# Performance work log

Measured on AMD Instinct MI355X. Metric: run time of the kernel, lower is better.

Reference implementation:

```python
import jax, jax.numpy as jnp
import numpy as np

B, S, D = 8, 4096, 1280   # batch, tokens, model width (== down_dim == out_dim)
R = 64                    # lora rank (mid_dim)
EMBED_W = D + R * R + D   # [down | mid | up] slices of the per-sample embed


def setup_inputs() -> dict:
    key = jax.random.key(0)
    ks = jax.random.split(key, 6)
    x = jax.random.normal(ks[0], (B, S, D), dtype=jnp.float32)
    embed = jax.random.normal(ks[1], (B, EMBED_W), dtype=jnp.float32) * 0.05
    w_down = jax.random.normal(ks[2], (R, D), dtype=jnp.float32) * 0.02
    b_down = jnp.zeros((R,), dtype=jnp.float32)
    w_up = jax.random.normal(ks[3], (D, R), dtype=jnp.float32) * 0.02
    b_up = jnp.zeros((D,), dtype=jnp.float32)
    return {"x": x, "embed": embed, "w_down": w_down, "b_down": b_down,
            "w_up": w_up, "b_up": b_up}


def reference(x, embed, w_down, b_down, w_up, b_up):
    # down_forward: modulate input channels by per-sample down weight, then lora_down
    down_w = embed[:, :D]                          # [B, D]
    h = x * down_w[:, None, :]                     # [B, S, D]
    h = jnp.einsum('bsd,rd->bsr', h, w_down) + b_down   # lora_down Linear(D->R)
    # mid_forward: per-sample [R,R] weight, x_chunk @ W.T  (batched, no python loop)
    mid_w = embed[:, D:D + R * R].reshape(B, R, R)       # [B, R, R]
    h = jnp.einsum('bsr,bqr->bsq', h, mid_w)             # [B, S, R]
    # up_forward: lora_up then modulate output channels by per-sample up weight
    out = jnp.einsum('bsr,dr->bsd', h, w_up) + b_up      # lora_up Linear(R->D)
    up_w = embed[:, -D:]                                 # [B, D]
    out = out * up_w[:, None, :]
    return out
```

## Files before the change

kernel.cpp:

```cpp
#include <hip/hip_runtime.h>

#define NB 8
#define NS 4096
#define ND 1280
#define NR 64
#define EW 6656

typedef __attribute__((ext_vector_type(4))) float f4;
typedef __attribute__((ext_vector_type(8))) short bf8;

__device__ __forceinline__ unsigned short f2bf(float f) {
  union { float f; unsigned u; } v; v.f = f;
  unsigned u = v.u + 0x7FFFu + ((v.u >> 16) & 1u);
  return (unsigned short)(u >> 16);
}

__global__ __launch_bounds__(256) void prep_all(const float* __restrict__ embed,
                                                const float* __restrict__ w_down,
                                                const float* __restrict__ w_up,
                                                const float* __restrict__ b_down,
                                                unsigned short* __restrict__ W2F,
                                                unsigned short* __restrict__ W3F,
                                                float* __restrict__ h2bias) {
  const int blk = blockIdx.x;
  const int t   = threadIdx.x;
  if (blk < 160) {
    const int b  = blk / 20;
    const int qg = (blk % 20) / 5;
    const int dg = blk % 5;
    __shared__ float mids[16][64];
    #pragma unroll
    for (int i = 0; i < 4; ++i) {
      int idx = t + i * 256;
      mids[idx >> 6][idx & 63] = embed[b * EW + ND + qg * 1024 + idx];
    }
    __syncthreads();
    const int d = dg * 256 + t;
    float acc[16];
    #pragma unroll
    for (int q = 0; q < 16; ++q) acc[q] = 0.f;
    for (int r = 0; r < 64; r += 8) {
      float wd[8];
      #pragma unroll
      for (int u = 0; u < 8; ++u) wd[u] = w_down[(r + u) * ND + d];
      #pragma unroll
      for (int u = 0; u < 8; ++u)
        #pragma unroll
        for (int q = 0; q < 16; ++q) acc[q] += mids[q][r + u] * wd[u];
    }
    const float dwn = embed[b * EW + d];
    const int kt = d >> 5, lanehi = (d & 31) >> 3, jj = d & 7;
    #pragma unroll
    for (int q = 0; q < 16; ++q)
      W2F[(((b * 40 + kt) * 4 + qg) << 9) + (lanehi * 16 + q) * 8 + jj] = f2bf(acc[q] * dwn);
  } else if (blk < 480) {
    int g = (blk - 160) * 256 + t;
    int d = g >> 6, q = g & 63;
    int kt = q >> 5, nt = d >> 4, lanei = ((q & 31) >> 3) * 16 + (d & 15), jj = q & 7;
    W3F[((kt * 80 + nt) * 64 + lanei) * 8 + jj] = f2bf(w_up[g]);
  } else {
    #pragma unroll
    for (int ii = 0; ii < 2; ++ii) {
      int id = ii * 256 + t;
      int bb = id >> 6, q = id & 63;
      float s = 0.f;
      for (int r = 0; r < 64; ++r) s += b_down[r] * embed[bb * EW + ND + q * 64 + r];
      h2bias[id] = s;
    }
  }
}

__global__ __launch_bounds__(256, 4) void fused_main(const float* __restrict__ x,
                                                     const float* __restrict__ embed,
                                                     const float* __restrict__ b_up,
                                                     const unsigned short* __restrict__ W2F,
                                                     const unsigned short* __restrict__ W3F,
                                                     const float* __restrict__ h2bias,
                                                     float* __restrict__ out) {
  const int tid  = threadIdx.x;
  const int lane = tid & 63;
  const int w    = tid >> 6;
  const int kh   = w >> 1;
  const int rt   = w & 1;
  const int b    = blockIdx.x & 7;
  const int tile = blockIdx.x >> 3;
  const int lo16 = lane & 15;
  const int hi4  = lane >> 4;
  const int wrow = tile * 32 + rt * 16;

  __shared__ __align__(16) char smem[32768 + 256];
  float (*xs)[2][1024]    = (float (*)[2][1024])smem;
  float (*h2p)[2][16][68] = (float (*)[2][16][68])smem;
  float* bias_s           = (float*)(smem + 32768);

  if (tid < 64) bias_s[tid] = h2bias[b * 64 + tid];

  const float* xbase = x + ((size_t)b * NS + wrow) * ND + kh * 640;
  const unsigned short* w2b = W2F + (size_t)b * 81920;

  #define ISSUE_DMA(ck, buf)                                                         \
    _Pragma("unroll")                                                                \
    for (int it = 0; it < 4; ++it) {                                                 \
      const int rloc = it * 4 + hi4;                                                 \
      const int cf   = lo16 ^ rloc;                                                  \
      const float* src = xbase + (size_t)rloc * ND + (ck) * 64 + cf * 4;             \
      __builtin_amdgcn_global_load_lds((__attribute__((address_space(1))) void*)src, \
          (__attribute__((address_space(3))) void*)&xs[w][buf][it * 256], 16, 0, 0); \
    }

  f4 acc[4] = {};
  bf8 bw[8];

  ISSUE_DMA(0, 0)
  {
    const unsigned short* wp = w2b + (((kh * 10) * 8) << 9) + lane * 8;
    #pragma unroll
    for (int i = 0; i < 8; ++i) bw[i] = *(const bf8*)(wp + (i << 9));
  }

  for (int ck = 0; ck < 10; ++ck) {
    const int buf = ck & 1;
    asm volatile("s_waitcnt vmcnt(0)" ::: "memory");
    const f4* xp = (const f4*)&xs[w][buf][0];
    f4 a0 = xp[lo16 * 16 + ((hi4 * 2)     ^ lo16)];
    f4 a1 = xp[lo16 * 16 + ((hi4 * 2 + 1) ^ lo16)];
    f4 a2 = xp[lo16 * 16 + ((hi4 * 2 + 8) ^ lo16)];
    f4 a3 = xp[lo16 * 16 + ((hi4 * 2 + 9) ^ lo16)];
    bf8 bn[8];
    const bool more = (ck < 9);
    if (more) {
      ISSUE_DMA(ck + 1, buf ^ 1)
      const unsigned short* wp = w2b + (size_t)(((kh * 10 + ck + 1) * 8) << 9) + lane * 8;
      #pragma unroll
      for (int i = 0; i < 8; ++i) bn[i] = *(const bf8*)(wp + (i << 9));
    }
    bf8 af0, af1;
    #pragma unroll
    for (int j = 0; j < 4; ++j) {
      af0[j]     = (short)f2bf(a0[j]);
      af0[4 + j] = (short)f2bf(a1[j]);
      af1[j]     = (short)f2bf(a2[j]);
      af1[4 + j] = (short)f2bf(a3[j]);
    }
    #pragma unroll
    for (int nt = 0; nt < 4; ++nt)
      acc[nt] = __builtin_amdgcn_mfma_f32_16x16x32_bf16(af0, bw[nt], acc[nt], 0, 0, 0);
    #pragma unroll
    for (int nt = 0; nt < 4; ++nt)
      acc[nt] = __builtin_amdgcn_mfma_f32_16x16x32_bf16(af1, bw[4 + nt], acc[nt], 0, 0, 0);
    if (more) {
      #pragma unroll
      for (int i = 0; i < 8; ++i) bw[i] = bn[i];
    }
  }

  __syncthreads();

  #pragma unroll
  for (int nt = 0; nt < 4; ++nt)
    #pragma unroll
    for (int j = 0; j < 4; ++j)
      h2p[kh][rt][hi4 * 4 + j][nt * 16 + lo16] = acc[nt][j];
  __syncthreads();

  const int row = lo16;
  f4 u0 = *(const f4*)&h2p[0][rt][row][hi4 * 8];
  f4 u1 = *(const f4*)&h2p[0][rt][row][hi4 * 8 + 4];
  f4 v0 = *(const f4*)&h2p[1][rt][row][hi4 * 8];
  f4 v1 = *(const f4*)&h2p[1][rt][row][hi4 * 8 + 4];
  f4 u2 = *(const f4*)&h2p[0][rt][row][32 + hi4 * 8];
  f4 u3 = *(const f4*)&h2p[0][rt][row][32 + hi4 * 8 + 4];
  f4 v2 = *(const f4*)&h2p[1][rt][row][32 + hi4 * 8];
  f4 v3 = *(const f4*)&h2p[1][rt][row][32 + hi4 * 8 + 4];
  bf8 ha0, ha1;
  #pragma unroll
  for (int j = 0; j < 4; ++j) {
    ha0[j]     = (short)f2bf(u0[j] + v0[j] + bias_s[hi4 * 8 + j]);
    ha0[4 + j] = (short)f2bf(u1[j] + v1[j] + bias_s[hi4 * 8 + 4 + j]);
    ha1[j]     = (short)f2bf(u2[j] + v2[j] + bias_s[32 + hi4 * 8 + j]);
    ha1[4 + j] = (short)f2bf(u3[j] + v3[j] + bias_s[32 + hi4 * 8 + 4 + j]);
  }

  const float* upw = embed + b * EW + (EW - ND);
  float* outp = out + ((size_t)b * NS + wrow + hi4 * 4) * ND;
  const int dt0 = kh * 40;
  bf8 b0 = *(const bf8*)(W3F + (size_t)(dt0 * 64 + lane) * 8);
  bf8 b1 = *(const bf8*)(W3F + (size_t)((80 + dt0) * 64 + lane) * 8);

  for (int i = 0; i < 40; ++i) {
    const int dt  = dt0 + i;
    const int pdt = (i < 39) ? dt + 1 : dt;
    bf8 nb0 = *(const bf8*)(W3F + (size_t)(pdt * 64 + lane) * 8);
    bf8 nb1 = *(const bf8*)(W3F + (size_t)((80 + pdt) * 64 + lane) * 8);
    f4 o = {};
    o = __builtin_amdgcn_mfma_f32_16x16x32_bf16(ha0, b0, o, 0, 0, 0);
    o = __builtin_amdgcn_mfma_f32_16x16x32_bf16(ha1, b1, o, 0, 0, 0);
    const int d = dt * 16 + lo16;
    const float scale = upw[d];
    const float bu = b_up[d];
    #pragma unroll
    for (int j = 0; j < 4; ++j)
      outp[(size_t)j * ND + d] = (o[j] + bu) * scale;
    b0 = nb0; b1 = nb1;
  }
}

extern "C" void kernel_launch(void* const* d_in, const int* in_sizes, int n_in,
                              void* d_out, int out_size, void* d_ws, size_t ws_size,
                              hipStream_t stream) {
  const float* x      = (const float*)d_in[0];
  const float* embed  = (const float*)d_in[1];
  const float* w_down = (const float*)d_in[2];
  const float* b_down = (const float*)d_in[3];
  const float* w_up   = (const float*)d_in[4];
  const float* b_up   = (const float*)d_in[5];
  float* out = (float*)d_out;

  unsigned short* W2F = (unsigned short*)d_ws;
  unsigned short* W3F = W2F + 8 * 40 * 4 * 512;
  float* h2bias = (float*)(W3F + 2 * 80 * 64 * 8);

  prep_all<<<481, 256, 0, stream>>>(embed, w_down, w_up, b_down, W2F, W3F, h2bias);
  fused_main<<<1024, 256, 0, stream>>>(x, embed, b_up, W2F, W3F, h2bias, out);
}
```

Before: 124.0 us.

## Split fused kernel into h2 projection and output kernels with coalesced stores

Splits the single fused kernel into two launches when workspace allows. The first computes the bf16 rank-64 intermediate and writes it to workspace. The second reloads it and runs the up-projection with transposed MFMA operands, staging results through LDS so each output row is written as coalesced 16-byte stores. It also swaps the hand-written bf16 rounding for packed float2-to-bf16 conversions. The aim is better store efficiency and occupancy for the write-heavy output phase, paid for with an extra launch and a workspace round trip for the intermediate.

```diff
diff --git a/kernel.cpp b/kernel.cpp
--- a/kernel.cpp
+++ b/kernel.cpp
@@ -1,4 +1,5 @@
 #include <hip/hip_runtime.h>
+#include <hip/hip_bf16.h>
 
 #define NB 8
 #define NS 4096
@@ -9,10 +10,17 @@
 typedef __attribute__((ext_vector_type(4))) float f4;
 typedef __attribute__((ext_vector_type(8))) short bf8;
 
+union BF8U { bf8 v; unsigned u[4]; };
+
 __device__ __forceinline__ unsigned short f2bf(float f) {
   union { float f; unsigned u; } v; v.f = f;
   unsigned u = v.u + 0x7FFFu + ((v.u >> 16) & 1u);
   return (unsigned short)(u >> 16);
+}
+
+__device__ __forceinline__ unsigned pk2(float a, float b) {
+  __hip_bfloat162 t = __float22bfloat162_rn(float2{a, b});
+  return *reinterpret_cast<unsigned*>(&t);
 }
 
 __global__ __launch_bounds__(256) void prep_all(const float* __restrict__ embed,
@@ -67,6 +75,185 @@
       for (int r = 0; r < 64; ++r) s += b_down[r] * embed[bb * EW + ND + q * 64 + r];
       h2bias[id] = s;
     }
+  }
+}
+
+__global__ __launch_bounds__(256) void k1_h2(const float* __restrict__ x,
+                                             const unsigned short* __restrict__ W2F,
+                                             const float* __restrict__ h2bias,
+                                             uint4* __restrict__ h2F) {
+  const int tid  = threadIdx.x;
+  const int lane = tid & 63;
+  const int w    = tid >> 6;
+  const int kh   = w >> 1;
+  const int rt   = w & 1;
+  const int b    = blockIdx.x & 7;
+  const int tile = blockIdx.x >> 3;
+  const int lo16 = lane & 15;
+  const int hi4  = lane >> 4;
+  const int wrow = tile * 32 + rt * 16;
+
+  __shared__ __align__(16) char smem[32768];
+  float (*xs)[2][1024]    = (float (*)[2][1024])smem;
+  float (*h2p)[2][16][68] = (float (*)[2][16][68])smem;
+
+  const float* xbase = x + ((size_t)b * NS + wrow) * ND + kh * 640;
+  const unsigned short* w2b = W2F + (size_t)b * 81920;
+
+  #define ISSUE_DMA(ck, buf)                                                         \
+    _Pragma("unroll")                                                                \
+    for (int it = 0; it < 4; ++it) {                                                 \
+      const int rloc = it * 4 + hi4;                                                 \
+      const int cf   = lo16 ^ rloc;                                                  \
+      const float* src = xbase + (size_t)rloc * ND + (ck) * 64 + cf * 4;             \
+      __builtin_amdgcn_global_load_lds((__attribute__((address_space(1))) void*)src, \
+          (__attribute__((address_space(3))) void*)&xs[w][buf][it * 256], 16, 0, 0); \
+    }
+
+  f4 acc[4] = {};
+  bf8 bw[8];
+
+  ISSUE_DMA(0, 0)
+  {
+    const unsigned short* wp = w2b + (((kh * 10) * 8) << 9) + lane * 8;
+    #pragma unroll
+    for (int i = 0; i < 8; ++i) bw[i] = *(const bf8*)(wp + (i << 9));
+  }
+
+  for (int ck = 0; ck < 10; ++ck) {
+    const int buf = ck & 1;
+    asm volatile("s_waitcnt vmcnt(0)" ::: "memory");
+    const f4* xp = (const f4*)&xs[w][buf][0];
+    f4 a0 = xp[lo16 * 16 + ((hi4 * 2)     ^ lo16)];
+    f4 a1 = xp[lo16 * 16 + ((hi4 * 2 + 1) ^ lo16)];
+    f4 a2 = xp[lo16 * 16 + ((hi4 * 2 + 8) ^ lo16)];
+    f4 a3 = xp[lo16 * 16 + ((hi4 * 2 + 9) ^ lo16)];
+    bf8 bn[8];
+    const bool more = (ck < 9);
+    if (more) {
+      ISSUE_DMA(ck + 1, buf ^ 1)
+      const unsigned short* wp = w2b + (size_t)(((kh * 10 + ck + 1) * 8) << 9) + lane * 8;
+      #pragma unroll
+      for (int i = 0; i < 8; ++i) bn[i] = *(const bf8*)(wp + (i << 9));
+    }
+    BF8U af0, af1;
+    af0.u[0] = pk2(a0[0], a0[1]); af0.u[1] = pk2(a0[2], a0[3]);
+    af0.u[2] = pk2(a1[0], a1[1]); af0.u[3] = pk2(a1[2], a1[3]);
+    af1.u[0] = pk2(a2[0], a2[1]); af1.u[1] = pk2(a2[2], a2[3]);
+    af1.u[2] = pk2(a3[0], a3[1]); af1.u[3] = pk2(a3[2], a3[3]);
+    #pragma unroll
+    for (int nt = 0; nt < 4; ++nt)
+      acc[nt] = __builtin_amdgcn_mfma_f32_16x16x32_bf16(af0.v, bw[nt], acc[nt], 0, 0, 0);
+    #pragma unroll
+    for (int nt = 0; nt < 4; ++nt)
+      acc[nt] = __builtin_amdgcn_mfma_f32_16x16x32_bf16(af1.v, bw[4 + nt], acc[nt], 0, 0, 0);
+    if (more) {
+      #pragma unroll
+      for (int i = 0; i < 8; ++i) bw[i] = bn[i];
+    }
+  }
+
+  __syncthreads();
+
+  #pragma unroll
+  for (int nt = 0; nt < 4; ++nt)
+    #pragma unroll
+    for (int j = 0; j < 4; ++j)
+      h2p[kh][rt][hi4 * 4 + j][nt * 16 + lo16] = acc[nt][j];
+  __syncthreads();
+
+  const int q0 = kh * 32 + hi4 * 8;
+  f4 u0 = *(const f4*)&h2p[0][rt][lo16][q0];
+  f4 u1 = *(const f4*)&h2p[0][rt][lo16][q0 + 4];
+  f4 v0 = *(const f4*)&h2p[1][rt][lo16][q0];
+  f4 v1 = *(const f4*)&h2p[1][rt][lo16][q0 + 4];
+  f4 c0 = *(const f4*)(h2bias + b * 64 + q0);
+  f4 c1 = *(const f4*)(h2bias + b * 64 + q0 + 4);
+  float s[8];
+  #pragma unroll
+  for (int j = 0; j < 4; ++j) {
+    s[j]     = u0[j] + v0[j] + c0[j];
+    s[4 + j] = u1[j] + v1[j] + c1[j];
+  }
+  uint4 pk;
+  pk.x = pk2(s[0], s[1]); pk.y = pk2(s[2], s[3]);
+  pk.z = pk2(s[4], s[5]); pk.w = pk2(s[6], s[7]);
+  h2F[(size_t)(((b * 256 + tile * 2 + rt) * 2 + kh) * 64 + lane)] = pk;
+}
+
+__global__ __launch_bounds__(256) void k2_out(const uint4* __restrict__ h2F,
+                                              const float* __restrict__ embed,
+                                              const float* __restrict__ b_up,
+                                              const unsigned short* __restrict__ W3F,
+                                              float* __restrict__ out) {
+  const int tid  = threadIdx.x;
+  const int lane = tid & 63;
+  const int w    = tid >> 6;
+  const int kh   = w >> 1;
+  const int rt   = w & 1;
+  const int b    = blockIdx.x & 7;
+  const int t2   = blockIdx.x >> 3;
+  const int lo16 = lane & 15;
+  const int hi4  = lane >> 4;
+
+  __shared__ __align__(16) float lds[4][16][68];
+
+  const int tile16 = t2 * 2 + rt;
+  uint4 hv0 = h2F[(size_t)(((b * 256 + tile16) * 2 + 0) * 64 + lane)];
+  uint4 hv1 = h2F[(size_t)(((b * 256 + tile16) * 2 + 1) * 64 + lane)];
+  BF8U ha0, ha1;
+  ha0.u[0] = hv0.x; ha0.u[1] = hv0.y; ha0.u[2] = hv0.z; ha0.u[3] = hv0.w;
+  ha1.u[0] = hv1.x; ha1.u[1] = hv1.y; ha1.u[2] = hv1.z; ha1.u[3] = hv1.w;
+
+  const int d0 = kh * 640;
+  const float* upw = embed + b * EW + (EW - ND) + d0;
+  const float* bup = b_up + d0;
+  float* outp = out + ((size_t)b * NS + t2 * 32 + rt * 16) * ND + d0;
+  const int dtbase = kh * 40;
+
+  bf8 wb[4][2];
+  #pragma unroll
+  for (int i = 0; i < 4; ++i) {
+    const int dt = dtbase + i;
+    wb[i][0] = *(const bf8*)(W3F + (size_t)(dt * 64 + lane) * 8);
+    wb[i][1] = *(const bf8*)(W3F + (size_t)((80 + dt) * 64 + lane) * 8);
+  }
+
+  for (int c = 0; c < 10; ++c) {
+    f4 o[4];
+    #pragma unroll
+    for (int i = 0; i < 4; ++i) {
+      f4 t = {};
+      t = __builtin_amdgcn_mfma_f32_16x16x32_bf16(wb[i][0], ha0.v, t, 0, 0, 0);
+      t = __builtin_amdgcn_mfma_f32_16x16x32_bf16(wb[i][1], ha1.v, t, 0, 0, 0);
+      o[i] = t;
+    }
+    bf8 wn[4][2];
+    if (c < 9) {
+      #pragma unroll
+      for (int i = 0; i < 4; ++i) {
+        const int dt = dtbase + (c + 1) * 4 + i;
+        wn[i][0] = *(const bf8*)(W3F + (size_t)(dt * 64 + lane) * 8);
+        wn[i][1] = *(const bf8*)(W3F + (size_t)((80 + dt) * 64 + lane) * 8);
+      }
+    }
+    #pragma unroll
+    for (int i = 0; i < 4; ++i) {
+      const int dl = c * 64 + i * 16 + hi4 * 4;
+      f4 sc = *(const f4*)(upw + dl);
+      f4 bu = *(const f4*)(bup + dl);
+      f4 r;
+      #pragma unroll
+      for (int j = 0; j < 4; ++j) r[j] = (o[i][j] + bu[j]) * sc[j];
+      *(f4*)&lds[w][lo16][i * 16 + hi4 * 4] = r;
+    }
+    #pragma unroll
+    for (int k = 0; k < 4; ++k) {
+      f4 v = *(const f4*)&lds[w][4 * k + hi4][lo16 * 4];
+      *(f4*)(outp + (size_t)(4 * k + hi4) * ND + c * 64 + lo16 * 4) = v;
+    }
+    #pragma unroll
+    for (int i = 0; i < 4; ++i) { wb[i][0] = wn[i][0]; wb[i][1] = wn[i][1]; }
   }
 }
 
@@ -98,26 +285,14 @@
   const float* xbase = x + ((size_t)b * NS + wrow) * ND + kh * 640;
   const unsigned short* w2b = W2F + (size_t)b * 81920;
 
-  #define ISSUE_DMA(ck, buf)                                                         \
-    _Pragma("unroll")                                                                \
-    for (int it = 0; it < 4; ++it) {                                                 \
-      const int rloc = it * 4 + hi4;                                                 \
-      const int cf   = lo16 ^ rloc;                                                  \
-      const float* src = xbase + (size_t)rloc * ND + (ck) * 64 + cf * 4;             \
-      __builtin_amdgcn_global_load_lds((__attribute__((address_space(1))) void*)src, \
-          (__attribute__((address_space(3))) void*)&xs[w][buf][it * 256], 16, 0, 0); \
-    }
-
   f4 acc[4] = {};
   bf8 bw[8];
-
   ISSUE_DMA(0, 0)
   {
     const unsigned short* wp = w2b + (((kh * 10) * 8) << 9) + lane * 8;
     #pragma unroll
     for (int i = 0; i < 8; ++i) bw[i] = *(const bf8*)(wp + (i << 9));
   }
-
   for (int ck = 0; ck < 10; ++ck) {
     const int buf = ck & 1;
     asm volatile("s_waitcnt vmcnt(0)" ::: "memory");
@@ -134,35 +309,29 @@
       #pragma unroll
       for (int i = 0; i < 8; ++i) bn[i] = *(const bf8*)(wp + (i << 9));
     }
-    bf8 af0, af1;
-    #pragma unroll
-    for (int j = 0; j < 4; ++j) {
-      af0[j]     = (short)f2bf(a0[j]);
-      af0[4 + j] = (short)f2bf(a1[j]);
-      af1[j]     = (short)f2bf(a2[j]);
-      af1[4 + j] = (short)f2bf(a3[j]);
-    }
+    BF8U af0, af1;
+    af0.u[0] = pk2(a0[0], a0[1]); af0.u[1] = pk2(a0[2], a0[3]);
+    af0.u[2] = pk2(a1[0], a1[1]); af0.u[3] = pk2(a1[2], a1[3]);
+    af1.u[0] = pk2(a2[0], a2[1]); af1.u[1] = pk2(a2[2], a2[3]);
+    af1.u[2] = pk2(a3[0], a3[1]); af1.u[3] = pk2(a3[2], a3[3]);
     #pragma unroll
     for (int nt = 0; nt < 4; ++nt)
-      acc[nt] = __builtin_amdgcn_mfma_f32_16x16x32_bf16(af0, bw[nt], acc[nt], 0, 0, 0);
+      acc[nt] = __builtin_amdgcn_mfma_f32_16x16x32_bf16(af0.v, bw[nt], acc[nt], 0, 0, 0);
     #pragma unroll
     for (int nt = 0; nt < 4; ++nt)
-      acc[nt] = __builtin_amdgcn_mfma_f32_16x16x32_bf16(af1, bw[4 + nt], acc[nt], 0, 0, 0);
+      acc[nt] = __builtin_amdgcn_mfma_f32_16x16x32_bf16(af1.v, bw[4 + nt], acc[nt], 0, 0, 0);
     if (more) {
       #pragma unroll
       for (int i = 0; i < 8; ++i) bw[i] = bn[i];
     }
   }
-
   __syncthreads();
-
   #pragma unroll
   for (int nt = 0; nt < 4; ++nt)
     #pragma unroll
     for (int j = 0; j < 4; ++j)
       h2p[kh][rt][hi4 * 4 + j][nt * 16 + lo16] = acc[nt][j];
   __syncthreads();
-
   const int row = lo16;
   f4 u0 = *(const f4*)&h2p[0][rt][row][hi4 * 8];
   f4 u1 = *(const f4*)&h2p[0][rt][row][hi4 * 8 + 4];
@@ -180,13 +349,11 @@
     ha1[j]     = (short)f2bf(u2[j] + v2[j] + bias_s[32 + hi4 * 8 + j]);
     ha1[4 + j] = (short)f2bf(u3[j] + v3[j] + bias_s[32 + hi4 * 8 + 4 + j]);
   }
-
   const float* upw = embed + b * EW + (EW - ND);
   float* outp = out + ((size_t)b * NS + wrow + hi4 * 4) * ND;
   const int dt0 = kh * 40;
   bf8 b0 = *(const bf8*)(W3F + (size_t)(dt0 * 64 + lane) * 8);
   bf8 b1 = *(const bf8*)(W3F + (size_t)((80 + dt0) * 64 + lane) * 8);
-
   for (int i = 0; i < 40; ++i) {
     const int dt  = dt0 + i;
     const int pdt = (i < 39) ? dt + 1 : dt;
@@ -216,10 +383,18 @@
   const float* b_up   = (const float*)d_in[5];
   float* out = (float*)d_out;
 
-  unsigned short* W2F = (unsigned short*)d_ws;
-  unsigned short* W3F = W2F + 8 * 40 * 4 * 512;
-  float* h2bias = (float*)(W3F + 2 * 80 * 64 * 8);
+  char* ws = (char*)d_ws;
+  unsigned short* W2F = (unsigned short*)ws;
+  unsigned short* W3F = (unsigned short*)(ws + 1310720);
+  float* h2bias       = (float*)(ws + 1474560);
+  uint4* h2F          = (uint4*)(ws + 1476608);
+  const size_t need   = 1476608 + 4194304;
 
   prep_all<<<481, 256, 0, stream>>>(embed, w_down, w_up, b_down, W2F, W3F, h2bias);
-  fused_main<<<1024, 256, 0, stream>>>(x, embed, b_up, W2F, W3F, h2bias, out);
-}
+  if (ws_size >= need) {
+    k1_h2 <<<1024, 256, 0, stream>>>(x, W2F, h2bias, h2F);
+    k2_out<<<1024, 256, 0, stream>>>(h2F, embed, b_up, W3F, out);
+  } else {
+    fused_main<<<1024, 256, 0, stream>>>(x, embed, b_up, W2F, W3F, h2bias, out);
+  }
+}
```

Result: faster. 104.9 us (-15.4%).

## Split fused kernel into h2 and output kernels with pre-scaled up weights

Applied to the files above, without the earlier changes.

Splits the single fused kernel into two: one computes the bf16 rank-64 intermediate and writes it to workspace, and one runs the up-projection. The per-sample up scale is folded into a per-batch bf16 copy of w_up during prep, and the up bias times scale is staged in LDS. Output tiles are transposed through LDS so each row is written as contiguous 128-byte segments, in place of scattered scalar stores. It also relaxes the DMA wait to vmcnt(12) for overlap and uses packed bf16 conversion. The cost is an extra launch, an intermediate round trip through global memory, and a larger prep kernel.

```diff
diff --git a/kernel.cpp b/kernel.cpp
--- a/kernel.cpp
+++ b/kernel.cpp
@@ -1,4 +1,5 @@
 #include <hip/hip_runtime.h>
+#include <hip/hip_bf16.h>
 
 #define NB 8
 #define NS 4096
@@ -9,10 +10,17 @@
 typedef __attribute__((ext_vector_type(4))) float f4;
 typedef __attribute__((ext_vector_type(8))) short bf8;
 
+union BF8U { bf8 v; unsigned u[4]; };
+
 __device__ __forceinline__ unsigned short f2bf(float f) {
   union { float f; unsigned u; } v; v.f = f;
   unsigned u = v.u + 0x7FFFu + ((v.u >> 16) & 1u);
   return (unsigned short)(u >> 16);
+}
+
+__device__ __forceinline__ unsigned pk2(float a, float b) {
+  __hip_bfloat162 t = __float22bfloat162_rn(float2{a, b});
+  return *reinterpret_cast<unsigned*>(&t);
 }
 
 __global__ __launch_bounds__(256) void prep_all(const float* __restrict__ embed,
@@ -20,7 +28,7 @@
                                                 const float* __restrict__ w_up,
                                                 const float* __restrict__ b_down,
                                                 unsigned short* __restrict__ W2F,
-                                                unsigned short* __restrict__ W3F,
+                                                unsigned short* __restrict__ W3FB,
                                                 float* __restrict__ h2bias) {
   const int blk = blockIdx.x;
   const int t   = threadIdx.x;
@@ -53,11 +61,15 @@
     #pragma unroll
     for (int q = 0; q < 16; ++q)
       W2F[(((b * 40 + kt) * 4 + qg) << 9) + (lanehi * 16 + q) * 8 + jj] = f2bf(acc[q] * dwn);
-  } else if (blk < 480) {
-    int g = (blk - 160) * 256 + t;
-    int d = g >> 6, q = g & 63;
-    int kt = q >> 5, nt = d >> 4, lanei = ((q & 31) >> 3) * 16 + (d & 15), jj = q & 7;
-    W3F[((kt * 80 + nt) * 64 + lanei) * 8 + jj] = f2bf(w_up[g]);
+  } else if (blk < 2720) {
+    const int local = blk - 160;
+    const int b  = local / 320;
+    const int g  = (local % 320) * 256 + t;
+    const int d  = g >> 6, q = g & 63;
+    const int kt = q >> 5, nt = d >> 4;
+    const int lanei = ((q & 31) >> 3) * 16 + (d & 15), jj = q & 7;
+    const float upw = embed[b * EW + 5376 + d];
+    W3FB[(size_t)b * 81920 + ((kt * 80 + nt) * 64 + lanei) * 8 + jj] = f2bf(w_up[g] * upw);
   } else {
     #pragma unroll
     for (int ii = 0; ii < 2; ++ii) {
@@ -70,13 +82,10 @@
   }
 }
 
-__global__ __launch_bounds__(256, 4) void fused_main(const float* __restrict__ x,
-                                                     const float* __restrict__ embed,
-                                                     const float* __restrict__ b_up,
-                                                     const unsigned short* __restrict__ W2F,
-                                                     const unsigned short* __restrict__ W3F,
-                                                     const float* __restrict__ h2bias,
-                                                     float* __restrict__ out) {
+__global__ __launch_bounds__(256, 4) void k1_h2(const float* __restrict__ x,
+                                                const unsigned short* __restrict__ W2F,
+                                                const float* __restrict__ h2bias,
+                                                uint4* __restrict__ h2F) {
   const int tid  = threadIdx.x;
   const int lane = tid & 63;
   const int w    = tid >> 6;
@@ -88,12 +97,9 @@
   const int hi4  = lane >> 4;
   const int wrow = tile * 32 + rt * 16;
 
-  __shared__ __align__(16) char smem[32768 + 256];
+  __shared__ __align__(16) char smem[32768];
   float (*xs)[2][1024]    = (float (*)[2][1024])smem;
   float (*h2p)[2][16][68] = (float (*)[2][16][68])smem;
-  float* bias_s           = (float*)(smem + 32768);
-
-  if (tid < 64) bias_s[tid] = h2bias[b * 64 + tid];
 
   const float* xbase = x + ((size_t)b * NS + wrow) * ND + kh * 640;
   const unsigned short* w2b = W2F + (size_t)b * 81920;
@@ -120,35 +126,33 @@
 
   for (int ck = 0; ck < 10; ++ck) {
     const int buf = ck & 1;
-    asm volatile("s_waitcnt vmcnt(0)" ::: "memory");
+    bf8 bn[8];
+    if (ck < 9) {
+      ISSUE_DMA(ck + 1, buf ^ 1)
+      const unsigned short* wp = w2b + (size_t)(((kh * 10 + ck + 1) * 8) << 9) + lane * 8;
+      #pragma unroll
+      for (int i = 0; i < 8; ++i) bn[i] = *(const bf8*)(wp + (i << 9));
+      asm volatile("s_waitcnt vmcnt(12)" ::: "memory");
+    } else {
+      asm volatile("s_waitcnt vmcnt(0)" ::: "memory");
+    }
     const f4* xp = (const f4*)&xs[w][buf][0];
     f4 a0 = xp[lo16 * 16 + ((hi4 * 2)     ^ lo16)];
     f4 a1 = xp[lo16 * 16 + ((hi4 * 2 + 1) ^ lo16)];
     f4 a2 = xp[lo16 * 16 + ((hi4 * 2 + 8) ^ lo16)];
     f4 a3 = xp[lo16 * 16 + ((hi4 * 2 + 9) ^ lo16)];
-    bf8 bn[8];
-    const bool more = (ck < 9);
-    if (more) {
-      ISSUE_DMA(ck + 1, buf ^ 1)
-      const unsigned short* wp = w2b + (size_t)(((kh * 10 + ck + 1) * 8) << 9) + lane * 8;
-      #pragma unroll
-      for (int i = 0; i < 8; ++i) bn[i] = *(const bf8*)(wp + (i << 9));
-    }
-    bf8 af0, af1;
-    #pragma unroll
-    for (int j = 0; j < 4; ++j) {
-      af0[j]     = (short)f2bf(a0[j]);
-      af0[4 + j] = (short)f2bf(a1[j]);
-      af1[j]     = (short)f2bf(a2[j]);
-      af1[4 + j] = (short)f2bf(a3[j]);
-    }
+    BF8U af0, af1;
+    af0.u[0] = pk2(a0[0], a0[1]); af0.u[1] = pk2(a0[2], a0[3]);
+    af0.u[2] = pk2(a1[0], a1[1]); af0.u[3] = pk2(a1[2], a1[3]);
+    af1.u[0] = pk2(a2[0], a2[1]); af1.u[1] = pk2(a2[2], a2[3]);
+    af1.u[2] = pk2(a3[0], a3[1]); af1.u[3] = pk2(a3[2], a3[3]);
     #pragma unroll
     for (int nt = 0; nt < 4; ++nt)
-      acc[nt] = __builtin_amdgcn_mfma_f32_16x16x32_bf16(af0, bw[nt], acc[nt], 0, 0, 0);
+      acc[nt] = __builtin_amdgcn_mfma_f32_16x16x32_bf16(af0.v, bw[nt], acc[nt], 0, 0, 0);
     #pragma unroll
     for (int nt = 0; nt < 4; ++nt)
-      acc[nt] = __builtin_amdgcn_mfma_f32_16x16x32_bf16(af1, bw[4 + nt], acc[nt], 0, 0, 0);
-    if (more) {
+      acc[nt] = __builtin_amdgcn_mfma_f32_16x16x32_bf16(af1.v, bw[4 + nt], acc[nt], 0, 0, 0);
+    if (ck < 9) {
       #pragma unroll
       for (int i = 0; i < 8; ++i) bw[i] = bn[i];
     }
@@ -163,45 +167,97 @@
       h2p[kh][rt][hi4 * 4 + j][nt * 16 + lo16] = acc[nt][j];
   __syncthreads();
 
-  const int row = lo16;
-  f4 u0 = *(const f4*)&h2p[0][rt][row][hi4 * 8];
-  f4 u1 = *(const f4*)&h2p[0][rt][row][hi4 * 8 + 4];
-  f4 v0 = *(const f4*)&h2p[1][rt][row][hi4 * 8];
-  f4 v1 = *(const f4*)&h2p[1][rt][row][hi4 * 8 + 4];
-  f4 u2 = *(const f4*)&h2p[0][rt][row][32 + hi4 * 8];
-  f4 u3 = *(const f4*)&h2p[0][rt][row][32 + hi4 * 8 + 4];
-  f4 v2 = *(const f4*)&h2p[1][rt][row][32 + hi4 * 8];
-  f4 v3 = *(const f4*)&h2p[1][rt][row][32 + hi4 * 8 + 4];
-  bf8 ha0, ha1;
+  const int q0 = kh * 32 + hi4 * 8;
+  f4 u0 = *(const f4*)&h2p[0][rt][lo16][q0];
+  f4 u1 = *(const f4*)&h2p[0][rt][lo16][q0 + 4];
+  f4 v0 = *(const f4*)&h2p[1][rt][lo16][q0];
+  f4 v1 = *(const f4*)&h2p[1][rt][lo16][q0 + 4];
+  f4 c0 = *(const f4*)(h2bias + b * 64 + q0);
+  f4 c1 = *(const f4*)(h2bias + b * 64 + q0 + 4);
+  float s[8];
   #pragma unroll
   for (int j = 0; j < 4; ++j) {
-    ha0[j]     = (short)f2bf(u0[j] + v0[j] + bias_s[hi4 * 8 + j]);
-    ha0[4 + j] = (short)f2bf(u1[j] + v1[j] + bias_s[hi4 * 8 + 4 + j]);
-    ha1[j]     = (short)f2bf(u2[j] + v2[j] + bias_s[32 + hi4 * 8 + j]);
-    ha1[4 + j] = (short)f2bf(u3[j] + v3[j] + bias_s[32 + hi4 * 8 + 4 + j]);
-  }
-
-  const float* upw = embed + b * EW + (EW - ND);
-  float* outp = out + ((size_t)b * NS + wrow + hi4 * 4) * ND;
-  const int dt0 = kh * 40;
-  bf8 b0 = *(const bf8*)(W3F + (size_t)(dt0 * 64 + lane) * 8);
-  bf8 b1 = *(const bf8*)(W3F + (size_t)((80 + dt0) * 64 + lane) * 8);
-
-  for (int i = 0; i < 40; ++i) {
-    const int dt  = dt0 + i;
-    const int pdt = (i < 39) ? dt + 1 : dt;
-    bf8 nb0 = *(const bf8*)(W3F + (size_t)(pdt * 64 + lane) * 8);
-    bf8 nb1 = *(const bf8*)(W3F + (size_t)((80 + pdt) * 64 + lane) * 8);
-    f4 o = {};
-    o = __builtin_amdgcn_mfma_f32_16x16x32_bf16(ha0, b0, o, 0, 0, 0);
-    o = __builtin_amdgcn_mfma_f32_16x16x32_bf16(ha1, b1, o, 0, 0, 0);
-    const int d = dt * 16 + lo16;
-    const float scale = upw[d];
-    const float bu = b_up[d];
-    #pragma unroll
-    for (int j = 0; j < 4; ++j)
-      outp[(size_t)j * ND + d] = (o[j] + bu) * scale;
-    b0 = nb0; b1 = nb1;
+    s[j]     = u0[j] + v0[j] + c0[j];
+    s[4 + j] = u1[j] + v1[j] + c1[j];
+  }
+  uint4 pk;
+  pk.x = pk2(s[0], s[1]); pk.y = pk2(s[2], s[3]);
+  pk.z = pk2(s[4], s[5]); pk.w = pk2(s[6], s[7]);
+  h2F[(size_t)(((b * 256 + tile * 2 + rt) * 2 + kh) * 64 + lane)] = pk;
+}
+
+__global__ __launch_bounds__(256, 4) void k2_out(const uint4* __restrict__ h2F,
+                                                 const float* __restrict__ embed,
+                                                 const float* __restrict__ b_up,
+                                                 const unsigned short* __restrict__ W3FB,
+                                                 float* __restrict__ out) {
+  const int tid  = threadIdx.x;
+  const int lane = tid & 63;
+  const int w    = tid >> 6;
+  const int kh   = w >> 1;
+  const int rt   = w & 1;
+  const int b    = blockIdx.x & 7;
+  const int t2   = blockIdx.x >> 3;
+  const int lo16 = lane & 15;
+  const int hi4  = lane >> 4;
+
+  __shared__ __align__(16) float lds[4][16][36];
+  __shared__ __align__(16) float pbs[1280];
+
+  const int tile16 = t2 * 2 + rt;
+  uint4 hv0 = h2F[(size_t)(((b * 256 + tile16) * 2 + 0) * 64 + lane)];
+  uint4 hv1 = h2F[(size_t)(((b * 256 + tile16) * 2 + 1) * 64 + lane)];
+
+  const float* upw = embed + b * EW + 5376;
+  #pragma unroll
+  for (int i = 0; i < 5; ++i) {
+    const int idx = i * 256 + tid;
+    pbs[idx] = b_up[idx] * upw[idx];
+  }
+  __syncthreads();
+
+  BF8U ha0, ha1;
+  ha0.u[0] = hv0.x; ha0.u[1] = hv0.y; ha0.u[2] = hv0.z; ha0.u[3] = hv0.w;
+  ha1.u[0] = hv1.x; ha1.u[1] = hv1.y; ha1.u[2] = hv1.z; ha1.u[3] = hv1.w;
+
+  const unsigned short* w3b = W3FB + (size_t)b * 81920;
+  float* outp = out + ((size_t)b * NS + t2 * 32 + rt * 16) * ND + kh * 640;
+  const int dtbase = kh * 40;
+
+  bf8 wb00 = *(const bf8*)(w3b + (size_t)((dtbase)      * 64 + lane) * 8);
+  bf8 wb01 = *(const bf8*)(w3b + (size_t)((80 + dtbase) * 64 + lane) * 8);
+  bf8 wb10 = *(const bf8*)(w3b + (size_t)((dtbase + 1)      * 64 + lane) * 8);
+  bf8 wb11 = *(const bf8*)(w3b + (size_t)((80 + dtbase + 1) * 64 + lane) * 8);
+
+  for (int c = 0; c < 20; ++c) {
+    f4 o0 = {}, o1 = {};
+    o0 = __builtin_amdgcn_mfma_f32_16x16x32_bf16(wb00, ha0.v, o0, 0, 0, 0);
+    o0 = __builtin_amdgcn_mfma_f32_16x16x32_bf16(wb01, ha1.v, o0, 0, 0, 0);
+    o1 = __builtin_amdgcn_mfma_f32_16x16x32_bf16(wb10, ha0.v, o1, 0, 0, 0);
+    o1 = __builtin_amdgcn_mfma_f32_16x16x32_bf16(wb11, ha1.v, o1, 0, 0, 0);
+    if (c < 19) {
+      const int dt = dtbase + (c + 1) * 2;
+      wb00 = *(const bf8*)(w3b + (size_t)(dt * 64 + lane) * 8);
+      wb01 = *(const bf8*)(w3b + (size_t)((80 + dt) * 64 + lane) * 8);
+      wb10 = *(const bf8*)(w3b + (size_t)((dt + 1) * 64 + lane) * 8);
+      wb11 = *(const bf8*)(w3b + (size_t)((80 + dt + 1) * 64 + lane) * 8);
+    }
+    #pragma unroll
+    for (int i = 0; i < 2; ++i) {
+      const f4 oi = i ? o1 : o0;
+      const int dl = kh * 640 + c * 32 + i * 16 + hi4 * 4;
+      f4 pbv = *(const f4*)&pbs[dl];
+      f4 r;
+      #pragma unroll
+      for (int j = 0; j < 4; ++j) r[j] = oi[j] + pbv[j];
+      *(f4*)&lds[w][lo16][i * 16 + hi4 * 4] = r;
+    }
+    #pragma unroll
+    for (int k = 0; k < 2; ++k) {
+      const int rr = k * 8 + (lane >> 3);
+      f4 v = *(const f4*)&lds[w][rr][(lane & 7) * 4];
+      *(f4*)(outp + (size_t)rr * ND + c * 32 + (lane & 7) * 4) = v;
+    }
   }
 }
 
@@ -216,10 +272,13 @@
   const float* b_up   = (const float*)d_in[5];
   float* out = (float*)d_out;
 
-  unsigned short* W2F = (unsigned short*)d_ws;
-  unsigned short* W3F = W2F + 8 * 40 * 4 * 512;
-  float* h2bias = (float*)(W3F + 2 * 80 * 64 * 8);
-
-  prep_all<<<481, 256, 0, stream>>>(embed, w_down, w_up, b_down, W2F, W3F, h2bias);
-  fused_main<<<1024, 256, 0, stream>>>(x, embed, b_up, W2F, W3F, h2bias, out);
-}
+  char* ws = (char*)d_ws;
+  unsigned short* W2F  = (unsigned short*)ws;
+  unsigned short* W3FB = (unsigned short*)(ws + 1310720);
+  float* h2bias        = (float*)(ws + 2621440);
+  uint4* h2F           = (uint4*)(ws + 2623488);
+
+  prep_all<<<2721, 256, 0, stream>>>(embed, w_down, w_up, b_down, W2F, W3FB, h2bias);
+  k1_h2   <<<1024, 256, 0, stream>>>(x, W2F, h2bias, h2F);
+  k2_out  <<<1024, 256, 0, stream>>>(h2F, embed, b_up, W3FB, out);
+}
```

Measured after the change: 102.9 us. -17.1%, faster.
